# Kernel tuning notes

Hardware: AMD Instinct MI355X
Metric: run time of the kernel (lower is better)

The kernel has to match this reference:

```python
import jax, jax.numpy as jnp
import numpy as np

NUM_EXPERTS = 8
HIDDEN_DIM = 2880
INTERMEDIATE_DIM = 2880
ALPHA = 1.702
LIMIT = 7.0
TOKENS = 2048


def _glorot(key, shape):
    fan_in, fan_out = shape[-2], shape[-1]
    limit = np.sqrt(6.0 / (fan_in + fan_out)).astype(np.float32)
    return jax.random.uniform(key, shape, jnp.float32, -limit, limit)


def setup_inputs() -> dict:
    key = jax.random.key(0)
    k1, k2, k3, k4 = jax.random.split(key, 4)
    hidden_states = jax.random.normal(k1, (TOKENS, HIDDEN_DIM), jnp.float32)
    rw = jax.random.uniform(k2, (TOKENS, NUM_EXPERTS), jnp.float32)
    routing_weights = rw / jnp.sum(rw, axis=-1, keepdims=True)
    gate_up_proj = _glorot(k3, (NUM_EXPERTS, HIDDEN_DIM, 2 * INTERMEDIATE_DIM))
    gate_up_bias = jnp.zeros((NUM_EXPERTS, 2 * INTERMEDIATE_DIM), jnp.float32)
    down_proj = _glorot(k4, (NUM_EXPERTS, INTERMEDIATE_DIM, HIDDEN_DIM))
    down_bias = jnp.zeros((NUM_EXPERTS, HIDDEN_DIM), jnp.float32)
    return {
        "hidden_states": hidden_states,
        "routing_weights": routing_weights,
        "gate_up_proj": gate_up_proj,
        "gate_up_bias": gate_up_bias,
        "down_proj": down_proj,
        "down_bias": down_bias,
    }


def reference(hidden_states, routing_weights, gate_up_proj, gate_up_bias, down_proj, down_bias):
    # [E, T, 2*I]
    gate_up = jnp.einsum("th,ehm->etm", hidden_states, gate_up_proj)
    gate_up = gate_up + gate_up_bias[:, None, :]
    gate = gate_up[..., ::2]   # interleaved gate channels
    up = gate_up[..., 1::2]    # interleaved up channels
    gate = jnp.minimum(gate, LIMIT)
    up = jnp.clip(up, -LIMIT, LIMIT)
    glu = gate * jax.nn.sigmoid(gate * ALPHA)
    gated = (up + 1.0) * glu                      # [E, T, I]
    expert_out = jnp.einsum("eti,eih->eth", gated, down_proj)
    expert_out = expert_out + down_bias[:, None, :]
    # weighted combine over experts: routing_weights [T, E] -> [E, T, 1]
    weighted = expert_out * routing_weights.T[:, :, None]
    return jnp.sum(weighted, axis=0)              # [T, H]
```

## Files before the change

### kernel.cpp

```cpp
#include <hip/hip_runtime.h>
#include <cstdint>
#include <cstddef>

#define TOK 2048
#define HID 2880
#define NI  2880
#define NG  5760
#define NE  8

typedef __attribute__((ext_vector_type(8))) short short8;
typedef __attribute__((ext_vector_type(4))) float f32x4;

__device__ __forceinline__ ushort f2bf(float f) {
  union { float f; uint32_t u; } v; v.f = f;
  uint32_t r = v.u + 0x7fffu + ((v.u >> 16) & 1u);
  return (ushort)(r >> 16);
}

#define GLOAD_LDS16(g, l)                                                           \
  __builtin_amdgcn_global_load_lds(                                                 \
      (const __attribute__((address_space(1))) void*)(g),                           \
      (__attribute__((address_space(3))) void*)(l), 16, 0, 0)

__global__ __launch_bounds__(256) void k_transpose(
    const float* __restrict__ in, ushort* __restrict__ out,
    int rows, int cols, int permHalf) {
  __shared__ float tile[64][65];
  const int e  = blockIdx.z;
  const int k0 = blockIdx.x * 64;
  const int n0 = blockIdx.y * 64;
  const size_t base = (size_t)e * rows * cols;
  const int t = threadIdx.x;
  const int r = t >> 2, q = t & 3;

  const float* src = in + base + (size_t)(k0 + r) * cols + n0;
#pragma unroll
  for (int j = 0; j < 4; ++j) {
    const int c = q * 4 + j * 16;
    const float4 v = *reinterpret_cast<const float4*>(src + c);
    tile[r][c + 0] = v.x; tile[r][c + 1] = v.y;
    tile[r][c + 2] = v.z; tile[r][c + 3] = v.w;
  }
  __syncthreads();

  const int n  = r;
  const int ks = q * 16;
  const int ng = n0 + n;
  const int row_out = permHalf ? ((ng & 1) ? (permHalf + (ng >> 1)) : (ng >> 1)) : ng;

  uint32_t pk[8];
#pragma unroll
  for (int j = 0; j < 8; ++j) {
    const ushort lo = f2bf(tile[ks + 2 * j][n]);
    const ushort hi = f2bf(tile[ks + 2 * j + 1][n]);
    pk[j] = ((uint32_t)hi << 16) | lo;
  }
  uint4* dst = (uint4*)(out + base + (size_t)row_out * rows + k0 + ks);
  dst[0] = make_uint4(pk[0], pk[1], pk[2], pk[3]);
  dst[1] = make_uint4(pk[4], pk[5], pk[6], pk[7]);
}

__global__ __launch_bounds__(256) void k_cvt_bf16(
    const float* __restrict__ in, ushort* __restrict__ out, int n8) {
  const int i = blockIdx.x * 256 + threadIdx.x;
  if (i < n8) {
    const float4 a = ((const float4*)in)[2 * i];
    const float4 b = ((const float4*)in)[2 * i + 1];
    uint4 o;
    o.x = ((uint32_t)f2bf(a.y) << 16) | f2bf(a.x);
    o.y = ((uint32_t)f2bf(a.w) << 16) | f2bf(a.z);
    o.z = ((uint32_t)f2bf(b.y) << 16) | f2bf(b.x);
    o.w = ((uint32_t)f2bf(b.w) << 16) | f2bf(b.z);
    ((uint4*)out)[i] = o;
  }
}

__global__ __launch_bounds__(256, 3) void k_gemm1(
    const ushort* __restrict__ A, const ushort* __restrict__ Wt,
    const float* __restrict__ bias, const float* __restrict__ rw,
    ushort* __restrict__ gated) {
  __shared__ __align__(16) short lds[16384];
  const int tid  = threadIdx.x;
  const int lane = tid & 63;
  const int wid  = tid >> 6;
  const int wm   = wid >> 1;
  const int wn   = wid & 1;

  const int bid = blockIdx.x;
  const int e   = bid & 7;
  const int rr  = bid >> 3;
  const int i0  = (rr >> 4) * 64;
  const int t0  = (rr & 15) * 128;

  const ushort* WtE = Wt + (size_t)e * NG * HID;

  const f32x4 fz = {0.f, 0.f, 0.f, 0.f};
  f32x4 accg[4][2], accu[4][2];
#pragma unroll
  for (int a = 0; a < 4; ++a)
#pragma unroll
    for (int b = 0; b < 2; ++b) { accg[a][b] = fz; accu[a][b] = fz; }

  const int lr  = lane >> 3;
  const int ks  = ((lane & 7) ^ lr) * 8;
  const int fr  = lane & 15;
  const int fg  = lane >> 4;
  const int fsw = lane & 7;

  for (int kk = 0; kk < HID; kk += 64) {
#pragma unroll
    for (int c = wid; c < 32; c += 4) {
      const ushort* src;
      if (c < 16)      src = A   + (size_t)(t0 + c * 8 + lr) * HID + kk + ks;
      else if (c < 24) src = WtE + (size_t)(i0 + (c - 16) * 8 + lr) * HID + kk + ks;
      else             src = WtE + (size_t)(NI + i0 + (c - 24) * 8 + lr) * HID + kk + ks;
      GLOAD_LDS16(src, &lds[c * 512]);
    }
    __syncthreads();

#pragma unroll
    for (int half = 0; half < 2; ++half) {
      const int ko = ((half * 4 + fg) ^ fsw) * 8;
      short8 af[4], bg[2], bu[2];
#pragma unroll
      for (int mi = 0; mi < 4; ++mi)
        af[mi] = *(const short8*)&lds[(wm * 64 + mi * 16 + fr) * 64 + ko];
#pragma unroll
      for (int ni = 0; ni < 2; ++ni) {
        bg[ni] = *(const short8*)&lds[8192  + (wn * 32 + ni * 16 + fr) * 64 + ko];
        bu[ni] = *(const short8*)&lds[12288 + (wn * 32 + ni * 16 + fr) * 64 + ko];
      }
#pragma unroll
      for (int mi = 0; mi < 4; ++mi)
#pragma unroll
        for (int ni = 0; ni < 2; ++ni) {
          accg[mi][ni] = __builtin_amdgcn_mfma_f32_16x16x32_bf16(af[mi], bg[ni], accg[mi][ni], 0, 0, 0);
          accu[mi][ni] = __builtin_amdgcn_mfma_f32_16x16x32_bf16(af[mi], bu[ni], accu[mi][ni], 0, 0, 0);
        }
    }
    __syncthreads();
  }

  float bg2[2], bu2[2];
  int iv[2];
#pragma unroll
  for (int ni = 0; ni < 2; ++ni) {
    iv[ni] = i0 + wn * 32 + ni * 16 + fr;
    bg2[ni] = bias[(size_t)e * NG + 2 * iv[ni]];
    bu2[ni] = bias[(size_t)e * NG + 2 * iv[ni] + 1];
  }
#pragma unroll
  for (int mi = 0; mi < 4; ++mi) {
#pragma unroll
    for (int j = 0; j < 4; ++j) {
      const int t = t0 + wm * 64 + mi * 16 + fg * 4 + j;
      const float rwv = rw[(size_t)t * NE + e];
#pragma unroll
      for (int ni = 0; ni < 2; ++ni) {
        float gate = accg[mi][ni][j] + bg2[ni];
        float up   = accu[mi][ni][j] + bu2[ni];
        gate = fminf(gate, 7.0f);
        up   = fminf(fmaxf(up, -7.0f), 7.0f);
        const float glu = gate / (1.0f + __expf(-1.702f * gate));
        gated[((size_t)e * TOK + t) * NI + iv[ni]] = f2bf(rwv * (up + 1.0f) * glu);
      }
    }
  }
}

__global__ __launch_bounds__(256, 3) void k_gemm2(
    const ushort* __restrict__ G, const ushort* __restrict__ Dt,
    const float* __restrict__ rw, const float* __restrict__ dbias,
    float* __restrict__ out) {
  __shared__ __align__(16) short lds[14336];
  const int tid  = threadIdx.x;
  const int lane = tid & 63;
  const int wid  = tid >> 6;
  const int wm   = wid >> 1;
  const int wn   = wid & 1;

  const int bid = blockIdx.x;
  const int swz = (bid & 7) * 60 + (bid >> 3);
  const int h0  = (swz >> 4) * 96;
  const int t0  = (swz & 15) * 128;

  const f32x4 fz = {0.f, 0.f, 0.f, 0.f};
  f32x4 acc[4][3];
#pragma unroll
  for (int a = 0; a < 4; ++a)
#pragma unroll
    for (int b = 0; b < 3; ++b) acc[a][b] = fz;

  const int lr  = lane >> 3;
  const int ks  = ((lane & 7) ^ lr) * 8;
  const int fr  = lane & 15;
  const int fg  = lane >> 4;
  const int fsw = lane & 7;

  for (int e = 0; e < NE; ++e) {
    const ushort* Ge = G  + (size_t)e * TOK * NI;
    const ushort* De = Dt + (size_t)e * HID * NI;

    for (int kk = 0; kk < NI; kk += 64) {
#pragma unroll
      for (int c = wid; c < 28; c += 4) {
        const ushort* src;
        if (c < 16) src = Ge + (size_t)(t0 + c * 8 + lr) * NI + kk + ks;
        else        src = De + (size_t)(h0 + (c - 16) * 8 + lr) * NI + kk + ks;
        GLOAD_LDS16(src, &lds[c * 512]);
      }
      __syncthreads();

#pragma unroll
      for (int half = 0; half < 2; ++half) {
        const int ko = ((half * 4 + fg) ^ fsw) * 8;
        short8 af[4], bf[3];
#pragma unroll
        for (int mi = 0; mi < 4; ++mi)
          af[mi] = *(const short8*)&lds[(wm * 64 + mi * 16 + fr) * 64 + ko];
#pragma unroll
        for (int ni = 0; ni < 3; ++ni)
          bf[ni] = *(const short8*)&lds[8192 + (wn * 48 + ni * 16 + fr) * 64 + ko];
#pragma unroll
        for (int mi = 0; mi < 4; ++mi)
#pragma unroll
          for (int ni = 0; ni < 3; ++ni)
            acc[mi][ni] = __builtin_amdgcn_mfma_f32_16x16x32_bf16(af[mi], bf[ni], acc[mi][ni], 0, 0, 0);
      }
      __syncthreads();
    }
  }

  int hv[3];
  float dbv[3][8];
#pragma unroll
  for (int ni = 0; ni < 3; ++ni) {
    hv[ni] = h0 + wn * 48 + ni * 16 + fr;
#pragma unroll
    for (int e = 0; e < 8; ++e)
      dbv[ni][e] = dbias[(size_t)e * HID + hv[ni]];
  }
#pragma unroll
  for (int mi = 0; mi < 4; ++mi) {
#pragma unroll
    for (int j = 0; j < 4; ++j) {
      const int t = t0 + wm * 64 + mi * 16 + fg * 4 + j;
      const float4 r0 = *(const float4*)(rw + (size_t)t * NE);
      const float4 r1 = *(const float4*)(rw + (size_t)t * NE + 4);
#pragma unroll
      for (int ni = 0; ni < 3; ++ni) {
        float s = acc[mi][ni][j];
        s += r0.x * dbv[ni][0] + r0.y * dbv[ni][1] + r0.z * dbv[ni][2] + r0.w * dbv[ni][3];
        s += r1.x * dbv[ni][4] + r1.y * dbv[ni][5] + r1.z * dbv[ni][6] + r1.w * dbv[ni][7];
        out[(size_t)t * HID + hv[ni]] = s;
      }
    }
  }
}

extern "C" void kernel_launch(void* const* d_in, const int* in_sizes, int n_in,
                              void* d_out, int out_size, void* d_ws, size_t ws_size,
                              hipStream_t stream) {
  const float* hs  = (const float*)d_in[0];
  const float* rw  = (const float*)d_in[1];
  const float* gup = (const float*)d_in[2];
  const float* gub = (const float*)d_in[3];
  const float* dwn = (const float*)d_in[4];
  const float* dnb = (const float*)d_in[5];
  float* out = (float*)d_out;

  char* ws = (char*)d_ws;
  ushort* gupT  = (ushort*)(ws);
  ushort* downT = (ushort*)(ws + 265420800u);
  ushort* hidB  = (ushort*)(ws + 265420800u + 132710400u);
  ushort* gated = (ushort*)(ws + 265420800u + 132710400u + 11796480u);

  k_transpose<<<dim3(HID / 64, NG / 64, NE), 256, 0, stream>>>(gup, gupT, HID, NG, NI);
  k_transpose<<<dim3(NI / 64, HID / 64, NE), 256, 0, stream>>>(dwn, downT, NI, HID, 0);
  k_cvt_bf16<<<(TOK * HID / 8 + 255) / 256, 256, 0, stream>>>(hs, hidB, TOK * HID / 8);
  k_gemm1<<<5760, 256, 0, stream>>>(hidB, gupT, gub, rw, gated);
  k_gemm2<<<480, 256, 0, stream>>>(gated, downT, rw, dnb, out);
}
```

Baseline: 1.859 ms.

## Split gemm2 expert reduction in two halves with wider N tiles and combine kernel

The down-projection GEMM grid is reorganized so each block covers 192 hidden columns instead of 96 and only four experts, with two expert halves running as separate blocks. Each half writes a partial result into a workspace buffer that reuses the gup transpose area, and a new elementwise kernel sums the two partials into the output. The goal is more A-tile reuse per LDS load and a shorter K-loop per block, at the cost of more registers and LDS per block plus an extra fp32 partial write, a readback, and one more launch.

```diff
diff --git a/kernel.cpp b/kernel.cpp
--- a/kernel.cpp
+++ b/kernel.cpp
@@ -171,8 +171,8 @@
 __global__ __launch_bounds__(256, 3) void k_gemm2(
     const ushort* __restrict__ G, const ushort* __restrict__ Dt,
     const float* __restrict__ rw, const float* __restrict__ dbias,
-    float* __restrict__ out) {
-  __shared__ __align__(16) short lds[14336];
+    float* __restrict__ partial) {
+  __shared__ __align__(16) short lds[20480];
   const int tid  = threadIdx.x;
   const int lane = tid & 63;
   const int wid  = tid >> 6;
@@ -181,15 +181,18 @@
 
   const int bid = blockIdx.x;
   const int swz = (bid & 7) * 60 + (bid >> 3);
-  const int h0  = (swz >> 4) * 96;
-  const int t0  = (swz & 15) * 128;
+  const int sid = (swz >= 240) ? 1 : 0;
+  const int r   = swz - sid * 240;
+  const int h0  = (r >> 4) * 192;
+  const int t0  = (r & 15) * 128;
+  const int e0  = sid * 4;
 
   const f32x4 fz = {0.f, 0.f, 0.f, 0.f};
-  f32x4 acc[4][3];
+  f32x4 acc[4][6];
 #pragma unroll
   for (int a = 0; a < 4; ++a)
 #pragma unroll
-    for (int b = 0; b < 3; ++b) acc[a][b] = fz;
+    for (int b = 0; b < 6; ++b) acc[a][b] = fz;
 
   const int lr  = lane >> 3;
   const int ks  = ((lane & 7) ^ lr) * 8;
@@ -197,13 +200,13 @@
   const int fg  = lane >> 4;
   const int fsw = lane & 7;
 
-  for (int e = 0; e < NE; ++e) {
-    const ushort* Ge = G  + (size_t)e * TOK * NI;
-    const ushort* De = Dt + (size_t)e * HID * NI;
+  for (int ee = 0; ee < 4; ++ee) {
+    const ushort* Ge = G  + (size_t)(e0 + ee) * TOK * NI;
+    const ushort* De = Dt + (size_t)(e0 + ee) * HID * NI;
 
     for (int kk = 0; kk < NI; kk += 64) {
 #pragma unroll
-      for (int c = wid; c < 28; c += 4) {
+      for (int c = wid; c < 40; c += 4) {
         const ushort* src;
         if (c < 16) src = Ge + (size_t)(t0 + c * 8 + lr) * NI + kk + ks;
         else        src = De + (size_t)(h0 + (c - 16) * 8 + lr) * NI + kk + ks;
@@ -214,47 +217,72 @@
 #pragma unroll
       for (int half = 0; half < 2; ++half) {
         const int ko = ((half * 4 + fg) ^ fsw) * 8;
-        short8 af[4], bf[3];
+        short8 af[4], bf[6];
 #pragma unroll
         for (int mi = 0; mi < 4; ++mi)
           af[mi] = *(const short8*)&lds[(wm * 64 + mi * 16 + fr) * 64 + ko];
 #pragma unroll
-        for (int ni = 0; ni < 3; ++ni)
-          bf[ni] = *(const short8*)&lds[8192 + (wn * 48 + ni * 16 + fr) * 64 + ko];
+        for (int ni = 0; ni < 6; ++ni)
+          bf[ni] = *(const short8*)&lds[8192 + (wn * 96 + ni * 16 + fr) * 64 + ko];
 #pragma unroll
         for (int mi = 0; mi < 4; ++mi)
 #pragma unroll
-          for (int ni = 0; ni < 3; ++ni)
+          for (int ni = 0; ni < 6; ++ni)
             acc[mi][ni] = __builtin_amdgcn_mfma_f32_16x16x32_bf16(af[mi], bf[ni], acc[mi][ni], 0, 0, 0);
       }
       __syncthreads();
     }
   }
 
-  int hv[3];
-  float dbv[3][8];
-#pragma unroll
-  for (int ni = 0; ni < 3; ++ni) {
-    hv[ni] = h0 + wn * 48 + ni * 16 + fr;
-#pragma unroll
-    for (int e = 0; e < 8; ++e)
-      dbv[ni][e] = dbias[(size_t)e * HID + hv[ni]];
-  }
-#pragma unroll
-  for (int mi = 0; mi < 4; ++mi) {
-#pragma unroll
-    for (int j = 0; j < 4; ++j) {
-      const int t = t0 + wm * 64 + mi * 16 + fg * 4 + j;
-      const float4 r0 = *(const float4*)(rw + (size_t)t * NE);
-      const float4 r1 = *(const float4*)(rw + (size_t)t * NE + 4);
-#pragma unroll
-      for (int ni = 0; ni < 3; ++ni) {
-        float s = acc[mi][ni][j];
-        s += r0.x * dbv[ni][0] + r0.y * dbv[ni][1] + r0.z * dbv[ni][2] + r0.w * dbv[ni][3];
-        s += r1.x * dbv[ni][4] + r1.y * dbv[ni][5] + r1.z * dbv[ni][6] + r1.w * dbv[ni][7];
-        out[(size_t)t * HID + hv[ni]] = s;
-      }
-    }
+  float* Pout = partial + (size_t)sid * TOK * HID;
+  int hv[6];
+#pragma unroll
+  for (int ni = 0; ni < 6; ++ni) hv[ni] = h0 + wn * 96 + ni * 16 + fr;
+
+  if (sid == 0) {
+#pragma unroll
+    for (int mi = 0; mi < 4; ++mi)
+#pragma unroll
+      for (int j = 0; j < 4; ++j) {
+        const int t = t0 + wm * 64 + mi * 16 + fg * 4 + j;
+#pragma unroll
+        for (int ni = 0; ni < 6; ++ni)
+          Pout[(size_t)t * HID + hv[ni]] = acc[mi][ni][j];
+      }
+  } else {
+    float dbv[6][8];
+#pragma unroll
+    for (int ni = 0; ni < 6; ++ni)
+#pragma unroll
+      for (int e = 0; e < 8; ++e)
+        dbv[ni][e] = dbias[(size_t)e * HID + hv[ni]];
+#pragma unroll
+    for (int mi = 0; mi < 4; ++mi)
+#pragma unroll
+      for (int j = 0; j < 4; ++j) {
+        const int t = t0 + wm * 64 + mi * 16 + fg * 4 + j;
+        const float4 r0 = *(const float4*)(rw + (size_t)t * NE);
+        const float4 r1 = *(const float4*)(rw + (size_t)t * NE + 4);
+#pragma unroll
+        for (int ni = 0; ni < 6; ++ni) {
+          float s = acc[mi][ni][j];
+          s += r0.x * dbv[ni][0] + r0.y * dbv[ni][1] + r0.z * dbv[ni][2] + r0.w * dbv[ni][3];
+          s += r1.x * dbv[ni][4] + r1.y * dbv[ni][5] + r1.z * dbv[ni][6] + r1.w * dbv[ni][7];
+          Pout[(size_t)t * HID + hv[ni]] = s;
+        }
+      }
+  }
+}
+
+__global__ __launch_bounds__(256) void k_combine(
+    const float* __restrict__ p, float* __restrict__ out, int n4) {
+  const int i = blockIdx.x * 256 + threadIdx.x;
+  if (i < n4) {
+    const float4 a = ((const float4*)p)[i];
+    const float4 b = ((const float4*)(p + (size_t)TOK * HID))[i];
+    float4 o;
+    o.x = a.x + b.x; o.y = a.y + b.y; o.z = a.z + b.z; o.w = a.w + b.w;
+    ((float4*)out)[i] = o;
   }
 }
 
@@ -274,10 +302,12 @@
   ushort* downT = (ushort*)(ws + 265420800u);
   ushort* hidB  = (ushort*)(ws + 265420800u + 132710400u);
   ushort* gated = (ushort*)(ws + 265420800u + 132710400u + 11796480u);
+  float*  part  = (float*)(ws);
 
   k_transpose<<<dim3(HID / 64, NG / 64, NE), 256, 0, stream>>>(gup, gupT, HID, NG, NI);
   k_transpose<<<dim3(NI / 64, HID / 64, NE), 256, 0, stream>>>(dwn, downT, NI, HID, 0);
   k_cvt_bf16<<<(TOK * HID / 8 + 255) / 256, 256, 0, stream>>>(hs, hidB, TOK * HID / 8);
   k_gemm1<<<5760, 256, 0, stream>>>(hidB, gupT, gub, rw, gated);
-  k_gemm2<<<480, 256, 0, stream>>>(gated, downT, rw, dnb, out);
-}
+  k_gemm2<<<480, 256, 0, stream>>>(gated, downT, rw, dnb, part);
+  k_combine<<<(TOK * HID / 4) / 256, 256, 0, stream>>>(part, out, TOK * HID / 4);
+}
```

After: 1.868 ms. No clear change (+0.5%).
